# Performance work log

Measured on AMD Instinct MI355X. Metric: run time of the kernel, lower is better.

## Reference

```python
import jax, jax.numpy as jnp
import numpy as np
from jax.scipy.special import gammaln

DIM = 64
N_FT = 1024
X_RANGE = 0.3
TWO_PI = 2.0 * np.pi


def gaussian_kernel_fun_ft(k, dim, scale_sq):
    # 1D Fourier coefficients of the sliced Gaussian kernel exp(-r^2/(2 sigma^2)):
    # f_hat(k) = pi^{d/2}/Gamma(d/2) * (2 pi sigma^2)^{d/2} * |k|^{d-1} * exp(-2 pi^2 sigma^2 k^2)
    # computed in log-space for stability at large d.
    logk = jnp.log(jnp.maximum(jnp.abs(k), 1e-30))
    log_f = (
        0.5 * dim * jnp.log(jnp.float32(np.pi))
        + 0.5 * dim * jnp.log(TWO_PI * scale_sq)
        - gammaln(jnp.float32(dim / 2.0))
        + (dim - 1) * logk
        - 2.0 * jnp.float32(np.pi**2) * scale_sq * k**2
    )
    return jnp.where(k == 0, jnp.float32(0.0), jnp.exp(log_f))


def setup_inputs() -> dict:
    key = jax.random.key(0)
    k1, k2, k3, k4 = jax.random.split(key, 4)
    N, M, P = 8192, 8192, 16
    return {
        "x": jax.random.normal(k1, (N, DIM), dtype=jnp.float32),
        "y": jax.random.normal(k2, (M, DIM), dtype=jnp.float32),
        "x_weights": jax.random.normal(k3, (N,), dtype=jnp.float32),
        "xis": jax.random.normal(k4, (P, DIM), dtype=jnp.float32),
        "scale": 10,
        "P": P,
    }


def reference(x, y, x_weights, xis, scale, P):
    # rescale all points into the ball of radius x_range (as fastsum_fft does)
    scale_f = jnp.float32(scale)
    max_norm = jnp.maximum(
        jnp.max(jnp.sqrt(jnp.sum(x**2, -1))), jnp.max(jnp.sqrt(jnp.sum(y**2, -1)))
    )
    sf = X_RANGE / max_norm
    xs = x * sf  # (N, d)
    ys = y * sf  # (M, d)
    s = scale_f * sf

    h = jnp.arange(-N_FT // 2, N_FT // 2, dtype=x.dtype)  # (K,) frequencies
    kft = gaussian_kernel_fun_ft(h, DIM, s**2)  # (K,)

    # get_xis: normalize random directions onto the unit sphere
    xis_n = xis / jnp.sqrt(jnp.sum(xis**2, -1, keepdims=True))  # (P, d)

    def body(acc, xi):
        xp = TWO_PI * (xs @ xi)  # (N,) projected source nodes, times 2*pi
        yp = TWO_PI * (ys @ xi)  # (M,)
        # adjoint NDFT: a_k = sum_i w_i e^{2 pi i k x_i}, split into real trig sums
        a_re = kft * (x_weights @ jnp.cos(xp[:, None] * h))  # (K,)
        a_im = kft * (x_weights @ jnp.sin(xp[:, None] * h))  # (K,)
        # forward NDFT at targets, real part of sum_k a_k kft_k e^{-2 pi i k y_j}
        out_p = jnp.cos(yp[:, None] * h) @ a_re + jnp.sin(yp[:, None] * h) @ a_im
        return acc + out_p, None

    acc, _ = jax.lax.scan(body, jnp.zeros(y.shape[0], x.dtype), xis_n)
    return acc / jnp.float32(xis_n.shape[0])  # average over the P slices
```

## Files before the change

kernel.cpp:

```cpp
#include <hip/hip_runtime.h>
#include <math.h>

#define DIM  64
#define PMX  16
#define KMX  16
#define POISON 0xAAAAAAAAu
#define FLAGV  0x5A5A5A5Au

#define WS_CNT0  0
#define WS_FLAG0 32
#define WS_CNT1  64
#define WS_FLAG1 96
#define WS_BMAX  128
#define WS_PART  192

__device__ __forceinline__ float aload(const float* p) {
    return __hip_atomic_load(p, __ATOMIC_RELAXED, __HIP_MEMORY_SCOPE_AGENT);
}
__device__ __forceinline__ void astore(float* p, float v) {
    __hip_atomic_store(p, v, __ATOMIC_RELAXED, __HIP_MEMORY_SCOPE_AGENT);
}

__device__ __forceinline__ void gbar(unsigned* cnt, unsigned* flag, unsigned nb) {
    __syncthreads();
    if (threadIdx.x == 0) {
        asm volatile("s_waitcnt vmcnt(0) lgkmcnt(0)" ::: "memory");
        unsigned old = __hip_atomic_fetch_add(cnt, 1u, __ATOMIC_RELAXED,
                                              __HIP_MEMORY_SCOPE_AGENT);
        if (old == POISON + nb - 1u) {
            __hip_atomic_store(flag, FLAGV, __ATOMIC_RELAXED, __HIP_MEMORY_SCOPE_AGENT);
        } else {
            for (int it = 0; it < (1 << 21); ++it) {
                if (__hip_atomic_load(flag, __ATOMIC_RELAXED,
                                      __HIP_MEMORY_SCOPE_AGENT) == FLAGV) break;
                __builtin_amdgcn_s_sleep(2);
            }
        }
    }
    __syncthreads();
}

__global__ void __launch_bounds__(256) k_main(
    const float* __restrict__ x, const float* __restrict__ y,
    const float* __restrict__ xw, const float* __restrict__ xis,
    const int* __restrict__ scale_raw, float* __restrict__ out,
    float* __restrict__ wsF, int N, int M, int P)
{
    __shared__ __align__(16) float sxi[PMX * DIM];
    __shared__ float sinv[PMX];
    __shared__ float sproj[256 * 17];
    __shared__ float sw[256];
    __shared__ float skft[KMX];
    __shared__ float sa[PMX * KMX * 2];
    __shared__ float s_sf_sh;
    __shared__ int   s_kmax;

    const int tid = threadIdx.x;
    const int bid = blockIdx.x;
    const int NXB = N >> 8, NYB = M >> 8;
    const unsigned NB = (unsigned)(NXB + NYB);
    const bool isx = bid < NXB;
    unsigned* bars = (unsigned*)wsF;

    for (int idx = tid * 4; idx < P * DIM; idx += blockDim.x * 4)
        *(float4*)(sxi + idx) = *(const float4*)(xis + idx);
    __syncthreads();
    if (tid < P) {
        float ss = 0.f;
        for (int d = 0; d < DIM; ++d) { float v = sxi[tid * DIM + d]; ss += v * v; }
        sinv[tid] = 1.0f / sqrtf(ss);
    }
    __syncthreads();

    const float* rbase = isx ? (x + ((size_t)bid * 256 + tid) * DIM)
                             : (y + ((size_t)(bid - NXB) * 256 + tid) * DIM);
    const float4* rowp = (const float4*)rbase;
    float ss = 0.f;
    float acc[PMX];
#pragma unroll
    for (int p = 0; p < PMX; ++p) acc[p] = 0.f;
#pragma unroll
    for (int d4 = 0; d4 < DIM / 4; ++d4) {
        float4 v = rowp[d4];
        ss += v.x * v.x + v.y * v.y + v.z * v.z + v.w * v.w;
#pragma unroll
        for (int p = 0; p < PMX; ++p) {
            float4 w = *(const float4*)(sxi + p * DIM + d4 * 4);
            acc[p] = fmaf(v.x, w.x, fmaf(v.y, w.y, fmaf(v.z, w.z, fmaf(v.w, w.w, acc[p]))));
        }
    }
#pragma unroll
    for (int p = 0; p < PMX; ++p) sproj[tid * 17 + p] = acc[p] * sinv[p];
    float mx = ss;
    for (int off = 32; off; off >>= 1) mx = fmaxf(mx, __shfl_down(mx, off));
    __shared__ float sred[4];
    if ((tid & 63) == 0) sred[tid >> 6] = mx;
    __syncthreads();
    if (tid == 0) {
        float m = fmaxf(fmaxf(sred[0], sred[1]), fmaxf(sred[2], sred[3]));
        astore(wsF + WS_BMAX + bid, m);
    }

    gbar(bars + WS_CNT0, bars + WS_FLAG0, NB);

    float m = (tid < (int)NB) ? aload(wsF + WS_BMAX + tid) : 0.f;
    for (int off = 32; off; off >>= 1) m = fmaxf(m, __shfl_down(m, off));
    if (tid == 0) { s_sf_sh = 0.3f / sqrtf(m); s_kmax = 0; }
    __syncthreads();
    const float sf = s_sf_sh;
    int iv = *scale_raw;
    float scale_f = (iv > -1000000 && iv < 1000000) ? (float)iv : __int_as_float(iv);
    float s2 = (scale_f * sf) * (scale_f * sf);
    if (tid < KMX) {
        int k = tid + 1;
        float kf = (float)k;
        const float C0 = 36.63135635f - 78.09222355f;
        float lf = C0 + 32.0f * logf(6.2831853071795864f * s2) + 63.0f * logf(kf)
                 - 19.739208802178716f * s2 * kf * kf;
        float kft = expf(lf);
        skft[tid] = kft;
        if (kft > 0.f) atomicMax(&s_kmax, k);
    }
    __syncthreads();
    const int kmax = min(s_kmax, KMX);

    if (isx) {
        sw[tid] = xw[bid * 256 + tid];
        __syncthreads();
        const int p = tid & 15, kk = tid >> 4;
        if (kk < kmax) {
            const float c1 = sf * (float)(kk + 1);
            float aRe = 0.f, aIm = 0.f;
            for (int i = 0; i < 256; ++i) {
                float pr = sproj[i * 17 + p];
                float w  = sw[i];
                float r = c1 * pr;
                r -= rintf(r);
                aRe = fmaf(w, __builtin_amdgcn_cosf(r), aRe);
                aIm = fmaf(w, __builtin_amdgcn_sinf(r), aIm);
            }
            float kf = skft[kk];
            int idx = (p * KMX + kk) * 2;
            astore(wsF + WS_PART + (size_t)idx * NXB + bid, aRe * kf);
            astore(wsF + WS_PART + (size_t)(idx + 1) * NXB + bid, aIm * kf);
        }
    }

    gbar(bars + WS_CNT1, bars + WS_FLAG1, NB);

    if (!isx) {
        for (int idx = tid; idx < PMX * KMX * 2; idx += blockDim.x) {
            int kk = (idx >> 1) & (KMX - 1);
            float s = 0.f;
            if (kk < kmax) {
                const float* pb = wsF + WS_PART + (size_t)idx * NXB;
                for (int c = 0; c < NXB; ++c) s += aload(pb + c);
            }
            sa[idx] = s;
        }
        __syncthreads();
        float accO = 0.f;
#pragma unroll
        for (int p = 0; p < PMX; ++p) {
            float bp = sf * sproj[tid * 17 + p];
            const float* ap = sa + p * KMX * 2;
            for (int kk = 0; kk < kmax; ++kk) {
                float r = bp * (float)(kk + 1);
                r -= rintf(r);
                accO = fmaf(__builtin_amdgcn_cosf(r), ap[2 * kk],     accO);
                accO = fmaf(__builtin_amdgcn_sinf(r), ap[2 * kk + 1], accO);
            }
        }
        out[(size_t)(bid - NXB) * 256 + tid] = accO * (2.0f / (float)P);
    }
}

extern "C" void kernel_launch(void* const* d_in, const int* in_sizes, int n_in,
                              void* d_out, int out_size, void* d_ws, size_t ws_size,
                              hipStream_t stream) {
    const float* x   = (const float*)d_in[0];
    const float* y   = (const float*)d_in[1];
    const float* xw  = (const float*)d_in[2];
    const float* xis = (const float*)d_in[3];
    const int* scale_raw = (const int*)d_in[4];
    float* wsF = (float*)d_ws;
    int N = in_sizes[0] / DIM;
    int M = in_sizes[1] / DIM;
    int P = in_sizes[3] / DIM;
    int NB = (N >> 8) + (M >> 8);

    k_main<<<NB, 256, 0, stream>>>(x, y, xw, xis, scale_raw,
                                   (float*)d_out, wsF, N, M, P);
}
```

Baseline: 96.10 us.

## Replace grid barriers with per-value poison polling and mixed x/y blocks

Drops the two counter-and-flag grid barriers. The launch shrinks to 64 blocks, and each block now projects 128 x rows and 128 y rows. Consumers spin on the individual workspace slots until the poison value is gone, so the block-max and partial-sum reads wait only on the data they need instead of a full grid barrier. Every block now both produces and consumes partials, and the y-side evaluation is split across two thread halves per target. The cost is far fewer blocks, each doing more serial trig work. Correctness also depends on the workspace being poisoned before every launch.

```diff
diff --git a/kernel.cpp b/kernel.cpp
--- a/kernel.cpp
+++ b/kernel.cpp
@@ -4,15 +4,11 @@
 #define DIM  64
 #define PMX  16
 #define KMX  16
+#define NB   64
 #define POISON 0xAAAAAAAAu
-#define FLAGV  0x5A5A5A5Au
 
-#define WS_CNT0  0
-#define WS_FLAG0 32
-#define WS_CNT1  64
-#define WS_FLAG1 96
-#define WS_BMAX  128
-#define WS_PART  192
+#define WS_BMAX  0
+#define WS_PART  64
 
 __device__ __forceinline__ float aload(const float* p) {
     return __hip_atomic_load(p, __ATOMIC_RELAXED, __HIP_MEMORY_SCOPE_AGENT);
@@ -20,24 +16,14 @@
 __device__ __forceinline__ void astore(float* p, float v) {
     __hip_atomic_store(p, v, __ATOMIC_RELAXED, __HIP_MEMORY_SCOPE_AGENT);
 }
-
-__device__ __forceinline__ void gbar(unsigned* cnt, unsigned* flag, unsigned nb) {
-    __syncthreads();
-    if (threadIdx.x == 0) {
-        asm volatile("s_waitcnt vmcnt(0) lgkmcnt(0)" ::: "memory");
-        unsigned old = __hip_atomic_fetch_add(cnt, 1u, __ATOMIC_RELAXED,
-                                              __HIP_MEMORY_SCOPE_AGENT);
-        if (old == POISON + nb - 1u) {
-            __hip_atomic_store(flag, FLAGV, __ATOMIC_RELAXED, __HIP_MEMORY_SCOPE_AGENT);
-        } else {
-            for (int it = 0; it < (1 << 21); ++it) {
-                if (__hip_atomic_load(flag, __ATOMIC_RELAXED,
-                                      __HIP_MEMORY_SCOPE_AGENT) == FLAGV) break;
-                __builtin_amdgcn_s_sleep(2);
-            }
-        }
+__device__ __forceinline__ float poll1(const float* p) {
+    float v = aload(p);
+    int it = 0;
+    while (__float_as_uint(v) == POISON && ++it < (1 << 20)) {
+        __builtin_amdgcn_s_sleep(1);
+        v = aload(p);
     }
-    __syncthreads();
+    return v;
 }
 
 __global__ void __launch_bounds__(256) k_main(
@@ -48,19 +34,20 @@
 {
     __shared__ __align__(16) float sxi[PMX * DIM];
     __shared__ float sinv[PMX];
-    __shared__ float sproj[256 * 17];
-    __shared__ float sw[256];
+    __shared__ float sprojx[128 * 17];
+    __shared__ float sprojy[128 * 17];
+    __shared__ float swx[128];
     __shared__ float skft[KMX];
     __shared__ float sa[PMX * KMX * 2];
+    __shared__ float sout[2 * 128];
+    __shared__ float sred[4];
     __shared__ float s_sf_sh;
     __shared__ int   s_kmax;
 
     const int tid = threadIdx.x;
     const int bid = blockIdx.x;
-    const int NXB = N >> 8, NYB = M >> 8;
-    const unsigned NB = (unsigned)(NXB + NYB);
-    const bool isx = bid < NXB;
-    unsigned* bars = (unsigned*)wsF;
+    const int XC = N / NB, YC = M / NB;
+    const bool isx = tid < XC;
 
     for (int idx = tid * 4; idx < P * DIM; idx += blockDim.x * 4)
         *(float4*)(sxi + idx) = *(const float4*)(xis + idx);
@@ -70,11 +57,11 @@
         for (int d = 0; d < DIM; ++d) { float v = sxi[tid * DIM + d]; ss += v * v; }
         sinv[tid] = 1.0f / sqrtf(ss);
     }
+    if (tid < XC) swx[tid] = xw[bid * XC + tid];
     __syncthreads();
 
-    const float* rbase = isx ? (x + ((size_t)bid * 256 + tid) * DIM)
-                             : (y + ((size_t)(bid - NXB) * 256 + tid) * DIM);
-    const float4* rowp = (const float4*)rbase;
+    const float4* rowp = (const float4*)(isx ? (x + ((size_t)bid * XC + tid) * DIM)
+                                             : (y + ((size_t)bid * YC + (tid - XC)) * DIM));
     float ss = 0.f;
     float acc[PMX];
 #pragma unroll
@@ -89,11 +76,13 @@
             acc[p] = fmaf(v.x, w.x, fmaf(v.y, w.y, fmaf(v.z, w.z, fmaf(v.w, w.w, acc[p]))));
         }
     }
+    {
+        float* dst = isx ? (sprojx + tid * 17) : (sprojy + (tid - XC) * 17);
 #pragma unroll
-    for (int p = 0; p < PMX; ++p) sproj[tid * 17 + p] = acc[p] * sinv[p];
+        for (int p = 0; p < PMX; ++p) dst[p] = acc[p] * sinv[p];
+    }
     float mx = ss;
     for (int off = 32; off; off >>= 1) mx = fmaxf(mx, __shfl_down(mx, off));
-    __shared__ float sred[4];
     if ((tid & 63) == 0) sred[tid >> 6] = mx;
     __syncthreads();
     if (tid == 0) {
@@ -101,11 +90,11 @@
         astore(wsF + WS_BMAX + bid, m);
     }
 
-    gbar(bars + WS_CNT0, bars + WS_FLAG0, NB);
-
-    float m = (tid < (int)NB) ? aload(wsF + WS_BMAX + tid) : 0.f;
-    for (int off = 32; off; off >>= 1) m = fmaxf(m, __shfl_down(m, off));
-    if (tid == 0) { s_sf_sh = 0.3f / sqrtf(m); s_kmax = 0; }
+    if (tid < 64) {
+        float m = (tid < NB) ? poll1(wsF + WS_BMAX + tid) : 0.f;
+        for (int off = 32; off; off >>= 1) m = fmaxf(m, __shfl_down(m, off));
+        if (tid == 0) { s_sf_sh = 0.3f / sqrtf(m); s_kmax = 0; }
+    }
     __syncthreads();
     const float sf = s_sf_sh;
     int iv = *scale_raw;
@@ -124,16 +113,14 @@
     __syncthreads();
     const int kmax = min(s_kmax, KMX);
 
-    if (isx) {
-        sw[tid] = xw[bid * 256 + tid];
-        __syncthreads();
+    {
         const int p = tid & 15, kk = tid >> 4;
         if (kk < kmax) {
             const float c1 = sf * (float)(kk + 1);
             float aRe = 0.f, aIm = 0.f;
-            for (int i = 0; i < 256; ++i) {
-                float pr = sproj[i * 17 + p];
-                float w  = sw[i];
+            for (int i = 0; i < XC; ++i) {
+                float pr = sprojx[i * 17 + p];
+                float w  = swx[i];
                 float r = c1 * pr;
                 r -= rintf(r);
                 aRe = fmaf(w, __builtin_amdgcn_cosf(r), aRe);
@@ -141,29 +128,43 @@
             }
             float kf = skft[kk];
             int idx = (p * KMX + kk) * 2;
-            astore(wsF + WS_PART + (size_t)idx * NXB + bid, aRe * kf);
-            astore(wsF + WS_PART + (size_t)(idx + 1) * NXB + bid, aIm * kf);
+            astore(wsF + WS_PART + (size_t)idx * NB + bid,       aRe * kf);
+            astore(wsF + WS_PART + (size_t)(idx + 1) * NB + bid, aIm * kf);
         }
     }
 
-    gbar(bars + WS_CNT1, bars + WS_FLAG1, NB);
+    for (int idx = tid; idx < PMX * KMX * 2; idx += blockDim.x) {
+        int kk = (idx >> 1) & (KMX - 1);
+        float s = 0.f;
+        if (kk < kmax) {
+            const float* pb = wsF + WS_PART + (size_t)idx * NB;
+            for (int base = 0; base < NB; base += 16) {
+                float v[16];
+#pragma unroll
+                for (int u = 0; u < 16; ++u) v[u] = aload(pb + base + u);
+#pragma unroll
+                for (int u = 0; u < 16; ++u) {
+                    if (__float_as_uint(v[u]) == POISON) v[u] = poll1(pb + base + u);
+                    s += v[u];
+                }
+            }
+        }
+        sa[idx] = s;
+    }
+    __syncthreads();
 
-    if (!isx) {
-        for (int idx = tid; idx < PMX * KMX * 2; idx += blockDim.x) {
-            int kk = (idx >> 1) & (KMX - 1);
-            float s = 0.f;
-            if (kk < kmax) {
-                const float* pb = wsF + WS_PART + (size_t)idx * NXB;
-                for (int c = 0; c < NXB; ++c) s += aload(pb + c);
-            }
-            sa[idx] = s;
-        }
-        __syncthreads();
+    {
+        const int j  = tid & 127;
+        const int ph = tid >> 7;
+        const int p0 = ph * 8;
         float accO = 0.f;
+        float bpv[8];
 #pragma unroll
-        for (int p = 0; p < PMX; ++p) {
-            float bp = sf * sproj[tid * 17 + p];
-            const float* ap = sa + p * KMX * 2;
+        for (int q = 0; q < 8; ++q) bpv[q] = sf * sprojy[j * 17 + p0 + q];
+#pragma unroll
+        for (int q = 0; q < 8; ++q) {
+            const float* ap = sa + ((p0 + q) * KMX) * 2;
+            float bp = bpv[q];
             for (int kk = 0; kk < kmax; ++kk) {
                 float r = bp * (float)(kk + 1);
                 r -= rintf(r);
@@ -171,7 +172,12 @@
                 accO = fmaf(__builtin_amdgcn_sinf(r), ap[2 * kk + 1], accO);
             }
         }
-        out[(size_t)(bid - NXB) * 256 + tid] = accO * (2.0f / (float)P);
+        sout[ph * 128 + j] = accO;
+    }
+    __syncthreads();
+    if (tid < YC) {
+        float v = (sout[tid] + sout[128 + tid]) * (2.0f / (float)P);
+        out[(size_t)bid * YC + tid] = v;
     }
 }
 
@@ -187,7 +193,6 @@
     int N = in_sizes[0] / DIM;
     int M = in_sizes[1] / DIM;
     int P = in_sizes[3] / DIM;
-    int NB = (N >> 8) + (M >> 8);
 
     k_main<<<NB, 256, 0, stream>>>(x, y, xw, xis, scale_raw,
                                    (float*)d_out, wsF, N, M, P);
```

After: 98.18 us, median of 2. 1.02x slower.
